# Optimization experiments

Measured on AMD Instinct MI355X. Metric: run time of the kernel, lower is better.

The kernel has to match this reference:

```python
import jax, jax.numpy as jnp
import numpy as np

B, S, E, H = 2, 2048, 1024, 16
D = E // H  # head_dim = 64
SCALE = D ** -0.5
NEG = -1e9


def setup_inputs() -> dict:
    key = jax.random.key(0)
    ks = jax.random.split(key, 10)
    hidden_states = jax.random.normal(ks[0], (B, S, E), dtype=jnp.float32)
    # CLIP-style additive causal mask [B, 1, L, S]
    causal = jnp.where(jnp.tril(jnp.ones((S, S), dtype=bool)), 0.0, NEG).astype(jnp.float32)
    attn_mask = jnp.broadcast_to(causal, (B, 1, S, S))
    def lin(kw, kb):
        W = jax.random.normal(kw, (E, E), dtype=jnp.float32) * (E ** -0.5)
        b = jax.random.normal(kb, (E,), dtype=jnp.float32) * 0.02
        return W, b
    Wq, bq = lin(ks[1], ks[2])
    Wk, bk = lin(ks[3], ks[4])
    Wv, bv = lin(ks[5], ks[6])
    Wo, bo = lin(ks[7], ks[8])
    return {"hidden_states": hidden_states, "attn_mask": attn_mask,
            "Wq": Wq, "bq": bq, "Wk": Wk, "bk": bk,
            "Wv": Wv, "bv": bv, "Wo": Wo, "bo": bo}


def reference(hidden_states, attn_mask, Wq, bq, Wk, bk, Wv, bv, Wo, bo):
    b, L, e = hidden_states.shape
    # projections (nn.Linear: x @ W.T + b)
    def split_heads(x):
        return x.reshape(b, L, H, D).transpose(0, 2, 1, 3)  # [b,h,l,d]
    q = split_heads(hidden_states @ Wq.T + bq)
    k = split_heads(hidden_states @ Wk.T + bk)
    v = split_heads(hidden_states @ Wv.T + bv)
    # QK^T * scale + additive mask, softmax, AV (dropout_p = 0 in eval)
    scores = jnp.einsum('bhld,bhsd->bhls', q, k) * SCALE + attn_mask
    attn = jax.nn.softmax(scores, axis=-1)
    ctx = jnp.einsum('bhls,bhsd->bhld', attn, v)
    ctx = ctx.transpose(0, 2, 1, 3).reshape(b, L, e)
    return ctx @ Wo.T + bo
```

## Files before the change

kernel.cpp:

```cpp
#include <hip/hip_runtime.h>
#include <hip/hip_bf16.h>
#include <stdint.h>


typedef __hip_bfloat16 bf16;
typedef short bf16x8 __attribute__((ext_vector_type(8)));
typedef short bf16x4 __attribute__((ext_vector_type(4)));
typedef float f32x4 __attribute__((ext_vector_type(4)));

__device__ __forceinline__ f32x4 mfma16(bf16x8 a, bf16x8 b, f32x4 c) {
  return __builtin_amdgcn_mfma_f32_16x16x32_bf16(a, b, c, 0, 0, 0);
}

__device__ __forceinline__ f32x4 mfma_k16(bf16x4 a, bf16x4 b, f32x4 c) {
#if __has_builtin(__builtin_amdgcn_mfma_f32_16x16x16bf16_1k)
  return __builtin_amdgcn_mfma_f32_16x16x16bf16_1k(a, b, c, 0, 0, 0);
#else
  f32x4 d;
  asm volatile("v_mfma_f32_16x16x16_bf16 %0, %1, %2, %3\n\ts_nop 7\n\ts_nop 7"
               : "=v"(d)
               : "v"(a), "v"(b), "v"(c));
  return d;
#endif
}

__device__ __forceinline__ void async16(const void* g, void* l) {
  __builtin_amdgcn_global_load_lds((const __attribute__((address_space(1))) void*)g,
                                   (__attribute__((address_space(3))) void*)l, 16, 0, 0);
}

__global__ __launch_bounds__(256) void cvt_kernel(
    const float* __restrict__ hs, const float* __restrict__ Wq,
    const float* __restrict__ Wk, const float* __restrict__ Wv,
    const float* __restrict__ Wo, bf16* __restrict__ dst) {
  const size_t e = ((size_t)blockIdx.x * 256 + threadIdx.x) * 8;
  const float* src;
  size_t off;
  if (e < 4194304) {
    src = hs; off = e;
  } else {
    const size_t w = e - 4194304;
    const int wi = (int)(w >> 20);
    src = (wi == 0) ? Wq : (wi == 1) ? Wk : (wi == 2) ? Wv : Wo;
    off = w & 1048575;
  }
  const float4 a = *(const float4*)(src + off);
  const float4 b = *(const float4*)(src + off + 4);
  union { bf16 h[8]; uint4 u; } p;
  p.h[0] = __float2bfloat16(a.x); p.h[1] = __float2bfloat16(a.y);
  p.h[2] = __float2bfloat16(a.z); p.h[3] = __float2bfloat16(a.w);
  p.h[4] = __float2bfloat16(b.x); p.h[5] = __float2bfloat16(b.y);
  p.h[6] = __float2bfloat16(b.z); p.h[7] = __float2bfloat16(b.w);
  *(uint4*)(dst + e) = p.u;
}

__global__ __launch_bounds__(256, 3) void qkv_gemm(
    const bf16* __restrict__ X, const bf16* __restrict__ Wb,
    const float* __restrict__ bq, const float* __restrict__ bk,
    const float* __restrict__ bv, bf16* __restrict__ out) {
  constexpr int Kd = 1024;
  __shared__ bf16 sA[2][128 * 32];
  __shared__ bf16 sB[2][128 * 32];
  const int tid = threadIdx.x;
  const int wave = tid >> 6, lane = tid & 63;
  const int g = lane >> 4, ln = lane & 15;
  const int tM = blockIdx.y * 128, tN = blockIdx.x * 128;
  const int which = tN >> 10;
  const bf16* W = Wb + (size_t)which * 1048576;
  const float* bias = (which == 0) ? bq : (which == 1) ? bk : bv;
  const int tNl = tN & 1023;
  const int wrow = (wave >> 1) * 64, wcol = (wave & 1) * 64;
  const f32x4 fz = {0.f, 0.f, 0.f, 0.f};

  f32x4 acc[4][4];
#pragma unroll
  for (int i = 0; i < 4; ++i)
#pragma unroll
    for (int j = 0; j < 4; ++j) acc[i][j] = fz;

  int srow[4], scol[4];
#pragma unroll
  for (int t = 0; t < 4; ++t) {
    const int d = tid + t * 256;
    srow[t] = (d >> 2) & 127;
    scol[t] = ((d >> 9) << 5) + ((d & 3) << 3);
  }

  for (int k0 = 0; k0 < Kd; k0 += 64) {
    __syncthreads();
#pragma unroll
    for (int t = 0; t < 4; ++t) {
      const int d = tid + t * 256;
      async16(X + (size_t)(tM + srow[t]) * Kd + k0 + scol[t], &sA[0][0] + d * 8);
      async16(W + (size_t)(tNl + srow[t]) * Kd + k0 + scol[t], &sB[0][0] + d * 8);
    }
    __syncthreads();
#pragma unroll
    for (int kk = 0; kk < 2; ++kk) {
      bf16x8 aF[4], bF[4];
#pragma unroll
      for (int i = 0; i < 4; ++i)
        aF[i] = *(const bf16x8*)(&sA[kk][0] + (wrow + i * 16 + ln) * 32 + g * 8);
#pragma unroll
      for (int j = 0; j < 4; ++j)
        bF[j] = *(const bf16x8*)(&sB[kk][0] + (wcol + j * 16 + ln) * 32 + g * 8);
#pragma unroll
      for (int i = 0; i < 4; ++i)
#pragma unroll
        for (int j = 0; j < 4; ++j) acc[i][j] = mfma16(aF[i], bF[j], acc[i][j]);
    }
  }

  bf16* outw = out + (size_t)which * 4194304;
  if (which == 2) {
    const int hh = (tNl + wcol) >> 6;
#pragma unroll
    for (int j = 0; j < 4; ++j) {
      const int nl = tNl + wcol + j * 16 + ln;
      const float bvf = bias[nl];
#pragma unroll
      for (int i = 0; i < 4; ++i) {
        const int m0 = tM + wrow + i * 16 + g * 4;
        const int b = m0 >> 11, t = (m0 & 2047) >> 6;
        union { bf16 hv[4]; bf16x4 v; } pk;
#pragma unroll
        for (int r = 0; r < 4; ++r) pk.hv[r] = __float2bfloat16(acc[i][j][r] + bvf);
        *(bf16x4*)(outw + (((size_t)(b * 16 + hh) * 32 + t) << 12) +
                   (i * 4 + j) * 256 + (g * 16 + ln) * 4) = pk.v;
      }
    }
  } else if (which == 1) {
    const int hh = (tNl + wcol) >> 6;
#pragma unroll
    for (int j = 0; j < 4; ++j) {
      const int nl = tNl + wcol + j * 16 + ln;
      const float bvf = bias[nl];
      const int half = j >> 1;
      const int gg = (j * 2 + (ln >> 3)) & 3;
      const int dl = ln & 7;
#pragma unroll
      for (int i = 0; i < 4; ++i) {
        const int m0 = tM + wrow + i * 16 + g * 4;
        const int b = m0 >> 11, t = (m0 & 2047) >> 6;
        bf16* basep = outw + (((size_t)(b * 16 + hh) * 32 + t) << 12) +
                      ((i * 2 + half) * 64 + gg * 16 + g * 4) * 8 + dl;
#pragma unroll
        for (int r = 0; r < 4; ++r)
          basep[r * 8] = __float2bfloat16(acc[i][j][r] + bvf);
      }
    }
  } else {
    const float oscale = 0.18033688011112042f;
#pragma unroll
    for (int j = 0; j < 4; ++j) {
      const int nl = tNl + wcol + j * 16 + ln;
      const float bvf = bias[nl];
      const int h = nl >> 6, d = nl & 63;
#pragma unroll
      for (int i = 0; i < 4; ++i) {
#pragma unroll
        for (int r = 0; r < 4; ++r) {
          const int m = tM + wrow + i * 16 + g * 4 + r;
          const int b = m >> 11, s = m & 2047;
          const float v = (acc[i][j][r] + bvf) * oscale;
          outw[(((size_t)(b * 16 + h) * 2048 + s) << 6) + d] = __float2bfloat16(v);
        }
      }
    }
  }
}

__global__ __launch_bounds__(256, 4) void out_gemm(
    const bf16* __restrict__ X, const bf16* __restrict__ W,
    const float* __restrict__ bias, float* __restrict__ out) {
  constexpr int Kd = 1024;
  __shared__ bf16 sA[64 * 32];
  __shared__ bf16 sB[64 * 32];
  const int tid = threadIdx.x;
  const int wave = tid >> 6, lane = tid & 63;
  const int g = lane >> 4, ln = lane & 15;
  const int tM = blockIdx.y * 64, tN = blockIdx.x * 64;
  const f32x4 fz = {0.f, 0.f, 0.f, 0.f};

  f32x4 acc[4];
#pragma unroll
  for (int j = 0; j < 4; ++j) acc[j] = fz;

  const int srow = tid >> 2, scol = (tid & 3) << 3;
  for (int k0 = 0; k0 < Kd; k0 += 32) {
    __syncthreads();
    async16(X + (size_t)(tM + srow) * Kd + k0 + scol, sA + tid * 8);
    async16(W + (size_t)(tN + srow) * Kd + k0 + scol, sB + tid * 8);
    __syncthreads();
    const bf16x8 aF = *(const bf16x8*)(sA + (wave * 16 + ln) * 32 + g * 8);
    bf16x8 bF[4];
#pragma unroll
    for (int j = 0; j < 4; ++j)
      bF[j] = *(const bf16x8*)(sB + (j * 16 + ln) * 32 + g * 8);
#pragma unroll
    for (int j = 0; j < 4; ++j) acc[j] = mfma16(aF, bF[j], acc[j]);
  }

#pragma unroll
  for (int j = 0; j < 4; ++j) {
    const int n = tN + j * 16 + ln;
    const float bvf = bias[n];
#pragma unroll
    for (int r = 0; r < 4; ++r) {
      const int m = tM + wave * 16 + g * 4 + r;
      out[(size_t)m * 1024 + n] = acc[j][r] + bvf;
    }
  }
}

__global__ __launch_bounds__(256, 4) void attn_kernel(
    const bf16* __restrict__ Q, const bf16* __restrict__ K,
    const bf16* __restrict__ V, bf16* __restrict__ O) {
  constexpr int S = 2048, D = 64;
  __shared__ bf16 sKf[2][4096];
  __shared__ bf16 sVf[2][4096];

  const int tid = threadIdx.x;
  const int w = tid >> 6, lane = tid & 63;
  const int g = lane >> 4, ln = lane & 15;
  const int px = blockIdx.x, py = blockIdx.y;
  const int bh = (px & 7) * 4 + (py & 3);
  const int s = py >> 3;
  const int q0 = (px >> 3) + 4 * ((py >> 2) & 1);
  const int qt = (s == 0) ? 31 - q0
               : (s == 1) ? 16 + q0
               : (s == 2) ? 15 - q0
                          : q0;
  const int b = bh >> 4, h = bh & 15;
  const f32x4 fz = {0.f, 0.f, 0.f, 0.f};

  const bf16* Qb = Q + (size_t)bh * S * D;
  const bf16* Kfb = K + (size_t)bh * 131072;
  const bf16* Vfb = V + (size_t)bh * 131072;

  bf16x8 qf[2];
#pragma unroll
  for (int kc = 0; kc < 2; ++kc)
    qf[kc] = *(const bf16x8*)(Qb + (size_t)(qt * 64 + w * 16 + ln) * D + kc * 32 + g * 8);

  f32x4 oacc[4];
#pragma unroll
  for (int db = 0; db < 4; ++db) oacc[db] = fz;
  f32x4 lacc = fz;
  const short onebf = (short)0x3F80;
  const bf16x4 onesf = {onebf, onebf, onebf, onebf};

  async16(Kfb + tid * 8, &sKf[0][0] + tid * 8);
  async16(Kfb + 2048 + tid * 8, &sKf[0][0] + 2048 + tid * 8);
  async16(Vfb + tid * 8, &sVf[0][0] + tid * 8);
  async16(Vfb + 2048 + tid * 8, &sVf[0][0] + 2048 + tid * 8);

  for (int kt = 0; kt <= qt; ++kt) {
    __syncthreads();
    if (kt < qt) {
      const bf16* ks = Kfb + (size_t)(kt + 1) * 4096;
      const bf16* vs = Vfb + (size_t)(kt + 1) * 4096;
      bf16* kb_ = &sKf[(kt + 1) & 1][0];
      bf16* vb_ = &sVf[(kt + 1) & 1][0];
      async16(ks + tid * 8, kb_ + tid * 8);
      async16(ks + 2048 + tid * 8, kb_ + 2048 + tid * 8);
      async16(vs + tid * 8, vb_ + tid * 8);
      async16(vs + 2048 + tid * 8, vb_ + 2048 + tid * 8);
    }
    const bf16* sKc = &sKf[kt & 1][0];
    const bf16* sVc = &sVf[kt & 1][0];

    f32x4 sacc[4];
#pragma unroll
    for (int kb = 0; kb < 4; ++kb) sacc[kb] = fz;
#pragma unroll
    for (int kb = 0; kb < 4; ++kb) {
      const bf16x8 k0 = *(const bf16x8*)(sKc + (kb * 2 + 0) * 512 + lane * 8);
      const bf16x8 k1 = *(const bf16x8*)(sKc + (kb * 2 + 1) * 512 + lane * 8);
      sacc[kb] = mfma16(k0, qf[0], sacc[kb]);
      sacc[kb] = mfma16(k1, qf[1], sacc[kb]);
    }

    const bool diag = (kt == qt);
    const int qloc = w * 16 + ln;
    bf16x4 pa[4];
#pragma unroll
    for (int kb = 0; kb < 4; ++kb) {
      union { bf16 hh[4]; bf16x4 v; } pu;
#pragma unroll
      for (int r = 0; r < 4; ++r) {
        float pv = exp2f(sacc[kb][r]);
        if (diag && (kb * 16 + g * 4 + r > qloc)) pv = 0.f;
        pu.hh[r] = __float2bfloat16(pv);
      }
      pa[kb] = pu.v;
      lacc = mfma_k16(pa[kb], onesf, lacc);
    }

#pragma unroll
    for (int db = 0; db < 4; ++db) {
#pragma unroll
      for (int kb = 0; kb < 4; ++kb) {
        const bf16x4 vf =
            *(const bf16x4*)(sVc + ((kb * 4 + db) * 64 + g * 16 + ln) * 4);
        oacc[db] = mfma_k16(pa[kb], vf, oacc[db]);
      }
    }
  }

  float invl[4];
#pragma unroll
  for (int r = 0; r < 4; ++r) invl[r] = 1.0f / lacc[r];

#pragma unroll
  for (int db = 0; db < 4; ++db)
#pragma unroll
    for (int r = 0; r < 4; ++r) {
      const int row = qt * 64 + w * 16 + g * 4 + r;
      const int col = db * 16 + ln;
      O[(((size_t)(b * 2048 + row) * 16 + h) << 6) + col] =
          __float2bfloat16(oacc[db][r] * invl[r]);
    }
}

extern "C" void kernel_launch(void* const* d_in, const int* in_sizes, int n_in,
                              void* d_out, int out_size, void* d_ws, size_t ws_size,
                              hipStream_t stream) {
  const float* hs = (const float*)d_in[0];
  const float* Wq = (const float*)d_in[2];
  const float* bq = (const float*)d_in[3];
  const float* Wk = (const float*)d_in[4];
  const float* bk = (const float*)d_in[5];
  const float* Wv = (const float*)d_in[6];
  const float* bv = (const float*)d_in[7];
  const float* Wo = (const float*)d_in[8];
  const float* bo = (const float*)d_in[9];
  float* out = (float*)d_out;

  char* ws = (char*)d_ws;
  bf16* XW = (bf16*)ws;
  bf16* Xb = XW;
  bf16* W3b = XW + 4194304;
  bf16* Wob = XW + 7340032;
  bf16* Qw = (bf16*)(ws + (16u << 20));
  bf16* Kw = (bf16*)(ws + (24u << 20));
  bf16* Vw = (bf16*)(ws + (32u << 20));
  bf16* Cw = (bf16*)ws;

  const dim3 blk(256);
  cvt_kernel<<<4096, blk, 0, stream>>>(hs, Wq, Wk, Wv, Wo, XW);
  qkv_gemm<<<dim3(24, 32), blk, 0, stream>>>(Xb, W3b, bq, bk, bv, Qw);
  attn_kernel<<<dim3(32, 32), blk, 0, stream>>>(Qw, Kw, Vw, Cw);
  out_gemm<<<dim3(16, 64), blk, 0, stream>>>(Cw, Wob, bo, out);
}
```

Before: 196.8 us.

## Split long causal query tiles across two blocks and merge partial results

Query tiles in the upper half of the causal range are now handled by two blocks. Each block covers half of the key tiles. The first half writes its unnormalized output to the context buffer, the second writes to a scratch buffer, and each stores its row sums. An atomic counter per pair lets the block that finishes last add the two partials and normalize. This shortens the longest per-block causal loop and balances work across a larger grid, at the cost of an extra memset, a partial-result round-trip through global memory, and extra bf16 rounding of the partials.

```diff
diff --git a/kernel.cpp b/kernel.cpp
--- a/kernel.cpp
+++ b/kernel.cpp
@@ -215,7 +215,9 @@
 
 __global__ __launch_bounds__(256, 4) void attn_kernel(
     const bf16* __restrict__ Q, const bf16* __restrict__ K,
-    const bf16* __restrict__ V, bf16* __restrict__ O) {
+    const bf16* __restrict__ V, bf16* __restrict__ O,
+    bf16* __restrict__ Phi, float* __restrict__ lLo,
+    float* __restrict__ lHi, unsigned int* __restrict__ flags) {
   constexpr int S = 2048, D = 64;
   __shared__ bf16 sKf[2][4096];
   __shared__ bf16 sVf[2][4096];
@@ -225,12 +227,23 @@
   const int g = lane >> 4, ln = lane & 15;
   const int px = blockIdx.x, py = blockIdx.y;
   const int bh = (px & 7) * 4 + (py & 3);
-  const int s = py >> 3;
-  const int q0 = (px >> 3) + 4 * ((py >> 2) & 1);
-  const int qt = (s == 0) ? 31 - q0
-               : (s == 1) ? 16 + q0
-               : (s == 2) ? 15 - q0
-                          : q0;
+  const int slot = (px >> 3) + 4 * (py >> 2);
+  int qt, k0t, k1t, pairid = 0, half = 0;
+  bool split;
+  if (slot < 32) {
+    split = true;
+    qt = 31 - (slot >> 1);
+    half = slot & 1;
+    const int nk = qt + 1, kl = (nk + 1) >> 1;
+    k0t = half ? kl : 0;
+    k1t = half ? nk : kl;
+    pairid = bh * 16 + (qt - 16);
+  } else {
+    split = false;
+    qt = 47 - slot;
+    k0t = 0;
+    k1t = qt + 1;
+  }
   const int b = bh >> 4, h = bh & 15;
   const f32x4 fz = {0.f, 0.f, 0.f, 0.f};
 
@@ -250,14 +263,20 @@
   const short onebf = (short)0x3F80;
   const bf16x4 onesf = {onebf, onebf, onebf, onebf};
 
-  async16(Kfb + tid * 8, &sKf[0][0] + tid * 8);
-  async16(Kfb + 2048 + tid * 8, &sKf[0][0] + 2048 + tid * 8);
-  async16(Vfb + tid * 8, &sVf[0][0] + tid * 8);
-  async16(Vfb + 2048 + tid * 8, &sVf[0][0] + 2048 + tid * 8);
-
-  for (int kt = 0; kt <= qt; ++kt) {
-    __syncthreads();
-    if (kt < qt) {
+  {
+    const bf16* ks = Kfb + (size_t)k0t * 4096;
+    const bf16* vs = Vfb + (size_t)k0t * 4096;
+    bf16* kb_ = &sKf[k0t & 1][0];
+    bf16* vb_ = &sVf[k0t & 1][0];
+    async16(ks + tid * 8, kb_ + tid * 8);
+    async16(ks + 2048 + tid * 8, kb_ + 2048 + tid * 8);
+    async16(vs + tid * 8, vb_ + tid * 8);
+    async16(vs + 2048 + tid * 8, vb_ + 2048 + tid * 8);
+  }
+
+  for (int kt = k0t; kt < k1t; ++kt) {
+    __syncthreads();
+    if (kt + 1 < k1t) {
       const bf16* ks = Kfb + (size_t)(kt + 1) * 4096;
       const bf16* vs = Vfb + (size_t)(kt + 1) * 4096;
       bf16* kb_ = &sKf[(kt + 1) & 1][0];
@@ -308,19 +327,71 @@
     }
   }
 
-  float invl[4];
-#pragma unroll
-  for (int r = 0; r < 4; ++r) invl[r] = 1.0f / lacc[r];
-
-#pragma unroll
-  for (int db = 0; db < 4; ++db)
-#pragma unroll
-    for (int r = 0; r < 4; ++r) {
-      const int row = qt * 64 + w * 16 + g * 4 + r;
-      const int col = db * 16 + ln;
-      O[(((size_t)(b * 2048 + row) * 16 + h) << 6) + col] =
-          __float2bfloat16(oacc[db][r] * invl[r]);
-    }
+  if (!split) {
+    float invl[4];
+#pragma unroll
+    for (int r = 0; r < 4; ++r) invl[r] = 1.0f / lacc[r];
+#pragma unroll
+    for (int db = 0; db < 4; ++db)
+#pragma unroll
+      for (int r = 0; r < 4; ++r) {
+        const int row = qt * 64 + w * 16 + g * 4 + r;
+        const int col = db * 16 + ln;
+        O[(((size_t)(b * 2048 + row) * 16 + h) << 6) + col] =
+            __float2bfloat16(oacc[db][r] * invl[r]);
+      }
+  } else {
+    if (half == 0) {
+#pragma unroll
+      for (int db = 0; db < 4; ++db)
+#pragma unroll
+        for (int r = 0; r < 4; ++r) {
+          const int row = qt * 64 + w * 16 + g * 4 + r;
+          const int col = db * 16 + ln;
+          O[(((size_t)(b * 2048 + row) * 16 + h) << 6) + col] =
+              __float2bfloat16(oacc[db][r]);
+        }
+    } else {
+#pragma unroll
+      for (int db = 0; db < 4; ++db)
+#pragma unroll
+        for (int r = 0; r < 4; ++r) {
+          const int rowloc = w * 16 + g * 4 + r;
+          const int col = db * 16 + ln;
+          Phi[((size_t)pairid * 64 + rowloc) * 64 + col] =
+              __float2bfloat16(oacc[db][r]);
+        }
+    }
+    if (ln == 0) {
+      float* lp = (half ? lHi : lLo) + pairid * 64 + w * 16 + g * 4;
+#pragma unroll
+      for (int r = 0; r < 4; ++r) lp[r] = lacc[r];
+    }
+    __threadfence();
+    int* sLast = (int*)&sKf[0][0];
+    if (tid == 0) *sLast = (atomicAdd(&flags[pairid], 1u) == 1u);
+    __syncthreads();
+    if (*sLast) {
+      __threadfence();
+      const int row = tid >> 2, c0 = (tid & 3) << 4;
+      const float li =
+          1.0f / (lLo[pairid * 64 + row] + lHi[pairid * 64 + row]);
+      const size_t cwo =
+          (((size_t)(b * 2048 + qt * 64 + row) * 16 + h) << 6) + c0;
+      const size_t pho = ((size_t)pairid * 64 + row) * 64 + c0;
+#pragma unroll
+      for (int h8 = 0; h8 < 2; ++h8) {
+        union { bf16 hh[8]; uint4 u; } ca, pb, ro;
+        ca.u = *(const uint4*)(O + cwo + h8 * 8);
+        pb.u = *(const uint4*)(Phi + pho + h8 * 8);
+#pragma unroll
+        for (int e = 0; e < 8; ++e)
+          ro.hh[e] = __float2bfloat16(
+              (__bfloat162float(ca.hh[e]) + __bfloat162float(pb.hh[e])) * li);
+        *(uint4*)(O + cwo + h8 * 8) = ro.u;
+      }
+    }
+  }
 }
 
 extern "C" void kernel_launch(void* const* d_in, const int* in_sizes, int n_in,
@@ -346,10 +417,16 @@
   bf16* Kw = (bf16*)(ws + (24u << 20));
   bf16* Vw = (bf16*)(ws + (32u << 20));
   bf16* Cw = (bf16*)ws;
+  bf16* Phi = (bf16*)(ws + 8388608);
+  float* lLo = (float*)(ws + 12582912);
+  float* lHi = (float*)(ws + 12582912 + 131072);
+  unsigned int* flags = (unsigned int*)(ws + 12582912 + 262144);
 
   const dim3 blk(256);
   cvt_kernel<<<4096, blk, 0, stream>>>(hs, Wq, Wk, Wv, Wo, XW);
   qkv_gemm<<<dim3(24, 32), blk, 0, stream>>>(Xb, W3b, bq, bk, bv, Qw);
-  attn_kernel<<<dim3(32, 32), blk, 0, stream>>>(Qw, Kw, Vw, Cw);
+  hipMemsetAsync(flags, 0, 2048, stream);
+  attn_kernel<<<dim3(32, 48), blk, 0, stream>>>(Qw, Kw, Vw, Cw,
+                                                Phi, lLo, lHi, flags);
   out_gemm<<<dim3(16, 64), blk, 0, stream>>>(Cw, Wob, bo, out);
 }
```

Measured after the change: 415.2 us. 111% more time.
